# Optimization experiments

Hardware: AMD Instinct MI355X
Metric: run time of the kernel (lower is better)

## Reference

```python
import jax, jax.numpy as jnp
import numpy as np

N_NODES = 20000
N_EDGES = 320000
N_GRAPHS = 64
IN_DIM = 39
HID = 128
HEADS = 4
NUM_CONV = 3
PRED_HID = 32
N_TASKS = 1
NEG_SLOPE = 0.2


def setup_inputs() -> dict:
    key = jax.random.key(0)
    ks = jax.random.split(key, 16)
    node_feat = jax.random.normal(ks[0], (N_NODES, IN_DIM), dtype=jnp.float32)
    edge_index = jax.random.randint(ks[1], (2, N_EDGES), 0, N_NODES, dtype=jnp.int64)
    batch = jnp.sort(jax.random.randint(ks[2], (N_NODES,), 0, N_GRAPHS, dtype=jnp.int64))
    s = 0.05
    return {
        "node_feat": node_feat,
        "edge_index": edge_index,
        "batch": batch,
        "emb_W": jax.random.normal(ks[3], (IN_DIM, HID), dtype=jnp.float32) * s,
        "emb_b": jnp.zeros((HID,), dtype=jnp.float32),
        "lin_W": jax.random.normal(ks[4], (NUM_CONV, HID, HEADS * HID), dtype=jnp.float32) * s,
        "att_src": jax.random.normal(ks[5], (NUM_CONV, HEADS, HID), dtype=jnp.float32) * s,
        "att_dst": jax.random.normal(ks[6], (NUM_CONV, HEADS, HID), dtype=jnp.float32) * s,
        "conv_b": jnp.zeros((NUM_CONV, HID), dtype=jnp.float32),
        "fc_W": jax.random.normal(ks[7], (HID, PRED_HID), dtype=jnp.float32) * s,
        "fc_b": jnp.zeros((PRED_HID,), dtype=jnp.float32),
        "out_W": jax.random.normal(ks[8], (PRED_HID, N_TASKS), dtype=jnp.float32) * s,
        "out_b": jnp.zeros((N_TASKS,), dtype=jnp.float32),
    }


def _gat_layer(x, src, dst, W, a_src, a_dst, b):
    # PyG GATConv (concat=False): per-head projection, additive attention,
    # segment softmax over incoming edges of each target node, head-mean + bias.
    N = x.shape[0]
    h = (x @ W).reshape(N, HEADS, HID)            # [N, H, F]
    a_s = jnp.einsum('nhf,hf->nh', h, a_src)       # [N, H]
    a_d = jnp.einsum('nhf,hf->nh', h, a_dst)       # [N, H]
    e = jax.nn.leaky_relu(a_s[src] + a_d[dst], NEG_SLOPE)   # [E, H]
    e_max = jax.ops.segment_max(e, dst, num_segments=N)      # [N, H]
    e = jnp.exp(e - e_max[dst])
    denom = jax.ops.segment_sum(e, dst, num_segments=N)      # [N, H]
    alpha = e / denom[dst]                                    # [E, H]
    msg = h[src] * alpha[..., None]                           # [E, H, F]
    out = jax.ops.segment_sum(msg, dst, num_segments=N)      # [N, H, F]
    return out.mean(axis=1) + b                               # [N, F]


def reference(node_feat, edge_index, batch, emb_W, emb_b, lin_W, att_src, att_dst,
              conv_b, fc_W, fc_b, out_W, out_b):
    N = node_feat.shape[0]
    loops = jnp.arange(N, dtype=edge_index.dtype)
    src = jnp.concatenate([edge_index[0], loops])  # add_self_loops=True
    dst = jnp.concatenate([edge_index[1], loops])

    x = node_feat @ emb_W + emb_b
    for l in range(NUM_CONV):
        x = _gat_layer(x, src, dst, lin_W[l], att_src[l], att_dst[l], conv_b[l])

    # global_mean_pool
    sums = jax.ops.segment_sum(x, batch, num_segments=N_GRAPHS)              # [G, F]
    cnt = jax.ops.segment_sum(jnp.ones((N,), x.dtype), batch, num_segments=N_GRAPHS)
    g = sums / jnp.maximum(cnt, 1.0)[:, None]

    g = g @ fc_W + fc_b
    return g @ out_W + out_b
```

## Files before the change

kernel.cpp:

```cpp
#include <hip/hip_runtime.h>
#include <math.h>

#define N_NODES 20000
#define E0      320000
#define E_TOT   (E0 + N_NODES)
#define N_GRAPHS 64
#define IN_DIM  39
#define HID     128
#define HEADS   4
#define HHID    (HEADS * HID)
#define NUM_CONV 3
#define PRED_HID 32
#define NEG_SLOPE 0.2f

__device__ __forceinline__ int esrc(const int* __restrict__ ei, int e) {
    return e < E0 ? ei[e] : (e - E0);
}
__device__ __forceinline__ int edst(const int* __restrict__ ei, int e) {
    return e < E0 ? ei[E0 + e] : (e - E0);
}

__global__ void k_deg(const int* __restrict__ ei, int* __restrict__ deg) {
    int e = blockIdx.x * blockDim.x + threadIdx.x;
    if (e >= E_TOT) return;
    atomicAdd(&deg[edst(ei, e)], 1);
}

__global__ __launch_bounds__(1024) void k_scan(const int* __restrict__ deg,
                                               int* __restrict__ row_ptr,
                                               int* __restrict__ cursor) {
    __shared__ int part[1024];
    const int CHUNK = 20;
    int t = threadIdx.x;
    int base = t * CHUNK;
    int s = 0;
    for (int i = 0; i < CHUNK; i++) {
        int idx = base + i;
        if (idx < N_NODES) s += deg[idx];
    }
    part[t] = s;
    __syncthreads();
    for (int off = 1; off < 1024; off <<= 1) {
        int v = (t >= off) ? part[t - off] : 0;
        __syncthreads();
        part[t] += v;
        __syncthreads();
    }
    int run = part[t] - s;
    for (int i = 0; i < CHUNK; i++) {
        int idx = base + i;
        if (idx < N_NODES) {
            row_ptr[idx] = run;
            cursor[idx]  = run;
            run += deg[idx];
        }
    }
    if (t == 1023) row_ptr[N_NODES] = part[1023];
}

__global__ void k_scatter(const int* __restrict__ ei, int* __restrict__ cursor,
                          int* __restrict__ csr_src) {
    int e = blockIdx.x * blockDim.x + threadIdx.x;
    if (e >= E_TOT) return;
    int d = edst(ei, e);
    int pos = atomicAdd(&cursor[d], 1);
    csr_src[pos] = esrc(ei, e);
}

__global__ __launch_bounds__(128) void k_emb(const float* __restrict__ nf,
                                             const float* __restrict__ W,
                                             const float* __restrict__ b,
                                             float* __restrict__ x) {
    __shared__ float f[IN_DIM];
    int n = blockIdx.x, t = threadIdx.x;
    if (t < IN_DIM) f[t] = nf[(size_t)n * IN_DIM + t];
    __syncthreads();
    float acc = b[t];
#pragma unroll
    for (int k = 0; k < IN_DIM; k++) acc += f[k] * W[k * HID + t];
    x[(size_t)n * HID + t] = acc;
}

__global__ __launch_bounds__(128) void k_wsd(const float* __restrict__ lin_W,
                                             const float* __restrict__ attS,
                                             const float* __restrict__ attD,
                                             float* __restrict__ Wsd) {
    int l = blockIdx.x >> 3, j = blockIdx.x & 7, k = threadIdx.x;
    int h = j & 3;
    const float* Wl = lin_W + (size_t)l * HID * HHID;
    const float* av = ((j < 4) ? attS : attD) + ((size_t)l * HEADS + h) * HID;
    const float* wr = Wl + (size_t)k * HHID + h * HID;
    float dot = 0.f;
#pragma unroll 4
    for (int f = 0; f < HID; f++) dot += wr[f] * av[f];
    Wsd[(size_t)l * 8 * HID + j * HID + k] = dot;
}

__global__ __launch_bounds__(256) void k_attproj(const float* __restrict__ x,
                                                 const float* __restrict__ WsdL,
                                                 float* __restrict__ A8) {
    __shared__ float sW[8 * HID];
    for (int i = threadIdx.x; i < 8 * HID; i += 256) sW[i] = WsdL[i];
    __syncthreads();
    int wid = threadIdx.x >> 6, lane = threadIdx.x & 63;
    int n = blockIdx.x * 4 + wid;
    if (n >= N_NODES) return;
    float2 xv = *(const float2*)(x + (size_t)n * HID + lane * 2);
    float p[8];
#pragma unroll
    for (int j = 0; j < 8; j++) {
        float v = xv.x * sW[j * HID + lane * 2] + xv.y * sW[j * HID + lane * 2 + 1];
#pragma unroll
        for (int off = 32; off; off >>= 1) v += __shfl_xor(v, off, 64);
        p[j] = v;
    }
    if (lane == 0) {
        *(float4*)(A8 + (size_t)n * 8)     = make_float4(p[0], p[1], p[2], p[3]);
        *(float4*)(A8 + (size_t)n * 8 + 4) = make_float4(p[4], p[5], p[6], p[7]);
    }
}

__global__ __launch_bounds__(256) void k_aggr(const float* __restrict__ x,
                                              const int* __restrict__ row_ptr,
                                              const int* __restrict__ csr_src,
                                              const float* __restrict__ A8,
                                              float* __restrict__ agg) {
    int wid = threadIdx.x >> 6, lane = threadIdx.x & 63;
    int n = blockIdx.x * 4 + wid;
    if (n >= N_NODES) return;
    float4 vd = *(const float4*)(A8 + (size_t)n * 8 + 4);
    int beg = row_ptr[n], end = row_ptr[n + 1];
    float a0x = 0.f, a0y = 0.f, a1x = 0.f, a1y = 0.f;
    float a2x = 0.f, a2y = 0.f, a3x = 0.f, a3y = 0.f;
    float d0 = 0.f, d1 = 0.f, d2 = 0.f, d3 = 0.f;
    int s_cur = (beg < end) ? csr_src[beg] : 0;
    for (int i = beg; i < end; i++) {
        int s_nx = (i + 1 < end) ? csr_src[i + 1] : 0;
        float4 vs = *(const float4*)(A8 + (size_t)s_cur * 8);
        float2 xv = *(const float2*)(x + (size_t)s_cur * HID + lane * 2);
        float v0 = vs.x + vd.x; v0 = fmaxf(v0, NEG_SLOPE * v0); float e0 = expf(v0);
        float v1 = vs.y + vd.y; v1 = fmaxf(v1, NEG_SLOPE * v1); float e1 = expf(v1);
        float v2 = vs.z + vd.z; v2 = fmaxf(v2, NEG_SLOPE * v2); float e2 = expf(v2);
        float v3 = vs.w + vd.w; v3 = fmaxf(v3, NEG_SLOPE * v3); float e3 = expf(v3);
        a0x += e0 * xv.x; a0y += e0 * xv.y;
        a1x += e1 * xv.x; a1y += e1 * xv.y;
        a2x += e2 * xv.x; a2y += e2 * xv.y;
        a3x += e3 * xv.x; a3y += e3 * xv.y;
        d0 += e0; d1 += e1; d2 += e2; d3 += e3;
        s_cur = s_nx;
    }
    float i0 = 1.f / d0, i1 = 1.f / d1, i2 = 1.f / d2, i3 = 1.f / d3;
    float* ag = agg + (size_t)n * HHID;
    *(float2*)(ag + 0 * HID + lane * 2) = make_float2(a0x * i0, a0y * i0);
    *(float2*)(ag + 1 * HID + lane * 2) = make_float2(a1x * i1, a1y * i1);
    *(float2*)(ag + 2 * HID + lane * 2) = make_float2(a2x * i2, a2y * i2);
    *(float2*)(ag + 3 * HID + lane * 2) = make_float2(a3x * i3, a3y * i3);
}

#define G2_BM 64
#define G2_KSPLIT 4
__global__ __launch_bounds__(256) void k_gemm2(const float* __restrict__ agg,
                                               const float* __restrict__ W,
                                               float* __restrict__ part, int M) {
    __shared__ float At[64][G2_BM];
    __shared__ float Bs[64][HID];
    int tid = threadIdx.x;
    int row0 = blockIdx.x * G2_BM;
    int ks = blockIdx.y;
    int ty = tid >> 4, tx = tid & 15;
    int r0 = ty * 4, c0 = tx * 4;
    float acc[4][8] = {};

#pragma unroll
    for (int kt = 0; kt < 2; kt++) {
        int kbase = ks * 128 + kt * 64;
        __syncthreads();
#pragma unroll
        for (int i = 0; i < 4; i++) {
            int idx = tid + i * 256;
            int r = idx >> 4;
            int c4 = idx & 15;
            int gr = row0 + r;
            float4 v = make_float4(0.f, 0.f, 0.f, 0.f);
            if (gr < M) v = *(const float4*)(agg + (size_t)gr * HHID + kbase + c4 * 4);
            int sw = (((r >> 2) ^ c4) << 2) + (r & 3);
            At[c4 * 4 + 0][sw] = v.x;
            At[c4 * 4 + 1][sw] = v.y;
            At[c4 * 4 + 2][sw] = v.z;
            At[c4 * 4 + 3][sw] = v.w;
        }
#pragma unroll
        for (int i = 0; i < 8; i++) {
            int idx = tid + i * 256;
            int kr = idx >> 5;
            int c4 = idx & 31;
            int kg = kbase + kr;
            int hd = kg >> 7, kk = kg & 127;
            *(float4*)(&Bs[kr][c4 * 4]) =
                *(const float4*)(W + (size_t)kk * HHID + hd * HID + c4 * 4);
        }
        __syncthreads();
#pragma unroll 4
        for (int k = 0; k < 64; k++) {
            float4 av = *(float4*)(&At[k][((ty ^ (k >> 2)) << 2)]);
            float4 b1 = *(float4*)(&Bs[k][c0]);
            float4 b2 = *(float4*)(&Bs[k][c0 + 64]);
            acc[0][0] += av.x * b1.x; acc[0][1] += av.x * b1.y; acc[0][2] += av.x * b1.z; acc[0][3] += av.x * b1.w;
            acc[0][4] += av.x * b2.x; acc[0][5] += av.x * b2.y; acc[0][6] += av.x * b2.z; acc[0][7] += av.x * b2.w;
            acc[1][0] += av.y * b1.x; acc[1][1] += av.y * b1.y; acc[1][2] += av.y * b1.z; acc[1][3] += av.y * b1.w;
            acc[1][4] += av.y * b2.x; acc[1][5] += av.y * b2.y; acc[1][6] += av.y * b2.z; acc[1][7] += av.y * b2.w;
            acc[2][0] += av.z * b1.x; acc[2][1] += av.z * b1.y; acc[2][2] += av.z * b1.z; acc[2][3] += av.z * b1.w;
            acc[2][4] += av.z * b2.x; acc[2][5] += av.z * b2.y; acc[2][6] += av.z * b2.z; acc[2][7] += av.z * b2.w;
            acc[3][0] += av.w * b1.x; acc[3][1] += av.w * b1.y; acc[3][2] += av.w * b1.z; acc[3][3] += av.w * b1.w;
            acc[3][4] += av.w * b2.x; acc[3][5] += av.w * b2.y; acc[3][6] += av.w * b2.z; acc[3][7] += av.w * b2.w;
        }
    }
    float* pb = part + (size_t)ks * M * HID;
#pragma unroll
    for (int i = 0; i < 4; i++) {
        int gr = row0 + r0 + i;
        if (gr < M) {
            *(float4*)(pb + (size_t)gr * HID + c0) =
                make_float4(acc[i][0], acc[i][1], acc[i][2], acc[i][3]);
            *(float4*)(pb + (size_t)gr * HID + c0 + 64) =
                make_float4(acc[i][4], acc[i][5], acc[i][6], acc[i][7]);
        }
    }
}

__global__ __launch_bounds__(256) void k_gfin(const float* __restrict__ part,
                                              const float* __restrict__ bias,
                                              const float* __restrict__ WsdL,
                                              float* __restrict__ xn,
                                              float* __restrict__ A8, int M) {
    __shared__ float sW[8 * HID];
    for (int i = threadIdx.x; i < 8 * HID; i += 256) sW[i] = WsdL[i];
    __syncthreads();
    int wid = threadIdx.x >> 6, lane = threadIdx.x & 63;
    int n = blockIdx.x * 4 + wid;
    if (n >= M) return;
    size_t off = (size_t)n * HID + lane * 2;
    size_t str = (size_t)M * HID;
    float2 p0 = *(const float2*)(part + off);
    float2 p1 = *(const float2*)(part + str + off);
    float2 p2 = *(const float2*)(part + 2 * str + off);
    float2 p3 = *(const float2*)(part + 3 * str + off);
    float2 bb = *(const float2*)(bias + lane * 2);
    float2 xv;
    xv.x = 0.25f * (p0.x + p1.x + p2.x + p3.x) + bb.x;
    xv.y = 0.25f * (p0.y + p1.y + p2.y + p3.y) + bb.y;
    *(float2*)(xn + off) = xv;
    float p[8];
#pragma unroll
    for (int j = 0; j < 8; j++) {
        float v = xv.x * sW[j * HID + lane * 2] + xv.y * sW[j * HID + lane * 2 + 1];
#pragma unroll
        for (int o = 32; o; o >>= 1) v += __shfl_xor(v, o, 64);
        p[j] = v;
    }
    if (lane == 0) {
        *(float4*)(A8 + (size_t)n * 8)     = make_float4(p[0], p[1], p[2], p[3]);
        *(float4*)(A8 + (size_t)n * 8 + 4) = make_float4(p[4], p[5], p[6], p[7]);
    }
}

#define POOL_NPB 64
__global__ __launch_bounds__(128) void k_pool(const float* __restrict__ x,
                                              const int* __restrict__ batch,
                                              float* __restrict__ g_sum,
                                              int* __restrict__ g_cnt) {
    int t = threadIdx.x;
    int n0 = blockIdx.x * POOL_NPB;
    int n1 = n0 + POOL_NPB; if (n1 > N_NODES) n1 = N_NODES;
    if (n0 >= n1) return;
    int cur = batch[n0];
    float acc = 0.f;
    int cnt = 0;
    for (int n = n0; n < n1; n++) {
        int b = batch[n];
        if (b != cur) {
            atomicAdd(&g_sum[cur * HID + t], acc);
            if (t == 0) atomicAdd(&g_cnt[cur], cnt);
            acc = 0.f; cnt = 0; cur = b;
        }
        acc += x[(size_t)n * HID + t];
        cnt++;
    }
    atomicAdd(&g_sum[cur * HID + t], acc);
    if (t == 0) atomicAdd(&g_cnt[cur], cnt);
}

__global__ __launch_bounds__(64) void k_head(const float* __restrict__ g_sum,
                                             const int* __restrict__ g_cnt,
                                             const float* __restrict__ fcW,
                                             const float* __restrict__ fcb,
                                             const float* __restrict__ outW,
                                             const float* __restrict__ outb,
                                             float* __restrict__ out) {
    int g = blockIdx.x, t = threadIdx.x;
    float inv = 1.f / fmaxf((float)g_cnt[g], 1.f);
    float val = 0.f;
    if (t < PRED_HID) {
        float dot = fcb[t];
        for (int f = 0; f < HID; f++)
            dot += (g_sum[g * HID + f] * inv) * fcW[f * PRED_HID + t];
        val = dot * outW[t];
    }
#pragma unroll
    for (int off = 32; off; off >>= 1) val += __shfl_xor(val, off, 64);
    if (t == 0) out[g] = val + outb[0];
}

extern "C" void kernel_launch(void* const* d_in, const int* in_sizes, int n_in,
                              void* d_out, int out_size, void* d_ws, size_t ws_size,
                              hipStream_t stream) {
    const float* node_feat = (const float*)d_in[0];
    const int*   edge_index = (const int*)d_in[1];
    const int*   batch     = (const int*)d_in[2];
    const float* emb_W     = (const float*)d_in[3];
    const float* emb_b     = (const float*)d_in[4];
    const float* lin_W     = (const float*)d_in[5];
    const float* att_src   = (const float*)d_in[6];
    const float* att_dst   = (const float*)d_in[7];
    const float* conv_b    = (const float*)d_in[8];
    const float* fc_W      = (const float*)d_in[9];
    const float* fc_b      = (const float*)d_in[10];
    const float* out_W     = (const float*)d_in[11];
    const float* out_b     = (const float*)d_in[12];
    float* out = (float*)d_out;

    char* p = (char*)d_ws;
    auto alloc = [&](size_t bytes) {
        void* r = (void*)p;
        p += (bytes + 255) & ~(size_t)255;
        return r;
    };
    float* x0      = (float*)alloc((size_t)N_NODES * HID * 4);
    float* x1      = (float*)alloc((size_t)N_NODES * HID * 4);
    float* agg     = (float*)alloc((size_t)N_NODES * HHID * 4);
    float* part    = (float*)alloc((size_t)G2_KSPLIT * N_NODES * HID * 4);
    float* A8      = (float*)alloc((size_t)N_NODES * 8 * 4);
    float* Wsd     = (float*)alloc((size_t)NUM_CONV * 8 * HID * 4);
    int*   deg     = (int*)alloc((size_t)(N_NODES + 1) * 4);
    int*   row_ptr = (int*)alloc((size_t)(N_NODES + 1) * 4);
    int*   cursor  = (int*)alloc((size_t)N_NODES * 4);
    int*   csr_src = (int*)alloc((size_t)E_TOT * 4);
    float* g_sum   = (float*)alloc((size_t)N_GRAPHS * HID * 4);
    int*   g_cnt   = (int*)alloc((size_t)N_GRAPHS * 4);

    const int EB = (E_TOT + 255) / 256;
    const int NB4 = (N_NODES + 3) / 4;

    hipMemsetAsync(deg, 0, (size_t)N_NODES * 4, stream);
    k_deg<<<EB, 256, 0, stream>>>(edge_index, deg);
    k_scan<<<1, 1024, 0, stream>>>(deg, row_ptr, cursor);
    k_scatter<<<EB, 256, 0, stream>>>(edge_index, cursor, csr_src);

    k_wsd<<<NUM_CONV * 8, 128, 0, stream>>>(lin_W, att_src, att_dst, Wsd);

    k_emb<<<N_NODES, 128, 0, stream>>>(node_feat, emb_W, emb_b, x0);
    k_attproj<<<NB4, 256, 0, stream>>>(x0, Wsd, A8);

    float* xin = x0;
    float* xout = x1;
    for (int l = 0; l < NUM_CONV; l++) {
        const float* Wl = lin_W + (size_t)l * HID * HHID;
        const float* bl = conv_b + (size_t)l * HID;
        int lnext = (l + 1 < NUM_CONV) ? l + 1 : NUM_CONV - 1;

        k_aggr<<<NB4, 256, 0, stream>>>(xin, row_ptr, csr_src, A8, agg);
        dim3 gg((N_NODES + G2_BM - 1) / G2_BM, G2_KSPLIT);
        k_gemm2<<<gg, 256, 0, stream>>>(agg, Wl, part, N_NODES);
        k_gfin<<<NB4, 256, 0, stream>>>(part, bl, Wsd + (size_t)lnext * 8 * HID,
                                        xout, A8, N_NODES);
        float* tmp = xin; xin = xout; xout = tmp;
    }

    hipMemsetAsync(g_sum, 0, (size_t)N_GRAPHS * HID * 4, stream);
    hipMemsetAsync(g_cnt, 0, (size_t)N_GRAPHS * 4, stream);
    k_pool<<<(N_NODES + POOL_NPB - 1) / POOL_NPB, 128, 0, stream>>>(xin, batch, g_sum, g_cnt);
    k_head<<<N_GRAPHS, 64, 0, stream>>>(g_sum, g_cnt, fc_W, fc_b,
                                        out_W, out_b, out);
}
```

Measured before the change: 480.3 us.

## Precompute per-edge attention exponentials in a separate edge kernel

Adds a per-edge kernel that computes the leaky-relu and exp of the attention logits once per edge per head and stores them in CSR order, using a new csr_dst array written during scatter. Before this, each of the 64 lanes in a wave computed those exps redundantly. The aggregation kernel now reads the precomputed values and prefetches the next edge's weights and source features one iteration ahead. The cost is an extra launch per layer plus writing and re-reading about 5 MB of edge weights.

New measurement: 456.4 us. 1.05x faster.

```diff
diff --git a/kernel.cpp b/kernel.cpp
--- a/kernel.cpp
+++ b/kernel.cpp
@@ -59,12 +59,13 @@
 }
 
 __global__ void k_scatter(const int* __restrict__ ei, int* __restrict__ cursor,
-                          int* __restrict__ csr_src) {
+                          int* __restrict__ csr_src, int* __restrict__ csr_dst) {
     int e = blockIdx.x * blockDim.x + threadIdx.x;
     if (e >= E_TOT) return;
     int d = edst(ei, e);
     int pos = atomicAdd(&cursor[d], 1);
     csr_src[pos] = esrc(ei, e);
+    csr_dst[pos] = d;
 }
 
 __global__ __launch_bounds__(128) void k_emb(const float* __restrict__ nf,
@@ -120,34 +121,54 @@
     }
 }
 
+__global__ void k_edge(const int* __restrict__ csr_src, const int* __restrict__ csr_dst,
+                       const float* __restrict__ A8, float* __restrict__ expE) {
+    int j = blockIdx.x * blockDim.x + threadIdx.x;
+    if (j >= E_TOT) return;
+    int s = csr_src[j], d = csr_dst[j];
+    float4 vs = *(const float4*)(A8 + (size_t)s * 8);
+    float4 vd = *(const float4*)(A8 + (size_t)d * 8 + 4);
+    float4 r;
+    float v;
+    v = vs.x + vd.x; v = fmaxf(v, NEG_SLOPE * v); r.x = expf(v);
+    v = vs.y + vd.y; v = fmaxf(v, NEG_SLOPE * v); r.y = expf(v);
+    v = vs.z + vd.z; v = fmaxf(v, NEG_SLOPE * v); r.z = expf(v);
+    v = vs.w + vd.w; v = fmaxf(v, NEG_SLOPE * v); r.w = expf(v);
+    *(float4*)(expE + (size_t)j * HEADS) = r;
+}
+
 __global__ __launch_bounds__(256) void k_aggr(const float* __restrict__ x,
                                               const int* __restrict__ row_ptr,
                                               const int* __restrict__ csr_src,
-                                              const float* __restrict__ A8,
+                                              const float* __restrict__ expE,
                                               float* __restrict__ agg) {
     int wid = threadIdx.x >> 6, lane = threadIdx.x & 63;
     int n = blockIdx.x * 4 + wid;
     if (n >= N_NODES) return;
-    float4 vd = *(const float4*)(A8 + (size_t)n * 8 + 4);
     int beg = row_ptr[n], end = row_ptr[n + 1];
     float a0x = 0.f, a0y = 0.f, a1x = 0.f, a1y = 0.f;
     float a2x = 0.f, a2y = 0.f, a3x = 0.f, a3y = 0.f;
     float d0 = 0.f, d1 = 0.f, d2 = 0.f, d3 = 0.f;
-    int s_cur = (beg < end) ? csr_src[beg] : 0;
+    float4 ep_nx = make_float4(0.f, 0.f, 0.f, 0.f);
+    float2 xv_nx = make_float2(0.f, 0.f);
+    if (beg < end) {
+        int s0 = csr_src[beg];
+        ep_nx = *(const float4*)(expE + (size_t)beg * HEADS);
+        xv_nx = *(const float2*)(x + (size_t)s0 * HID + lane * 2);
+    }
     for (int i = beg; i < end; i++) {
-        int s_nx = (i + 1 < end) ? csr_src[i + 1] : 0;
-        float4 vs = *(const float4*)(A8 + (size_t)s_cur * 8);
-        float2 xv = *(const float2*)(x + (size_t)s_cur * HID + lane * 2);
-        float v0 = vs.x + vd.x; v0 = fmaxf(v0, NEG_SLOPE * v0); float e0 = expf(v0);
-        float v1 = vs.y + vd.y; v1 = fmaxf(v1, NEG_SLOPE * v1); float e1 = expf(v1);
-        float v2 = vs.z + vd.z; v2 = fmaxf(v2, NEG_SLOPE * v2); float e2 = expf(v2);
-        float v3 = vs.w + vd.w; v3 = fmaxf(v3, NEG_SLOPE * v3); float e3 = expf(v3);
-        a0x += e0 * xv.x; a0y += e0 * xv.y;
-        a1x += e1 * xv.x; a1y += e1 * xv.y;
-        a2x += e2 * xv.x; a2y += e2 * xv.y;
-        a3x += e3 * xv.x; a3y += e3 * xv.y;
-        d0 += e0; d1 += e1; d2 += e2; d3 += e3;
-        s_cur = s_nx;
+        float4 ep = ep_nx;
+        float2 xv = xv_nx;
+        if (i + 1 < end) {
+            int s2 = csr_src[i + 1];
+            ep_nx = *(const float4*)(expE + (size_t)(i + 1) * HEADS);
+            xv_nx = *(const float2*)(x + (size_t)s2 * HID + lane * 2);
+        }
+        a0x += ep.x * xv.x; a0y += ep.x * xv.y;
+        a1x += ep.y * xv.x; a1y += ep.y * xv.y;
+        a2x += ep.z * xv.x; a2y += ep.z * xv.y;
+        a3x += ep.w * xv.x; a3y += ep.w * xv.y;
+        d0 += ep.x; d1 += ep.y; d2 += ep.z; d3 += ep.w;
     }
     float i0 = 1.f / d0, i1 = 1.f / d1, i2 = 1.f / d2, i3 = 1.f / d3;
     float* ag = agg + (size_t)n * HHID;
@@ -341,10 +362,12 @@
     float* part    = (float*)alloc((size_t)G2_KSPLIT * N_NODES * HID * 4);
     float* A8      = (float*)alloc((size_t)N_NODES * 8 * 4);
     float* Wsd     = (float*)alloc((size_t)NUM_CONV * 8 * HID * 4);
+    float* expE    = (float*)alloc((size_t)E_TOT * HEADS * 4);
     int*   deg     = (int*)alloc((size_t)(N_NODES + 1) * 4);
     int*   row_ptr = (int*)alloc((size_t)(N_NODES + 1) * 4);
     int*   cursor  = (int*)alloc((size_t)N_NODES * 4);
     int*   csr_src = (int*)alloc((size_t)E_TOT * 4);
+    int*   csr_dst = (int*)alloc((size_t)E_TOT * 4);
     float* g_sum   = (float*)alloc((size_t)N_GRAPHS * HID * 4);
     int*   g_cnt   = (int*)alloc((size_t)N_GRAPHS * 4);
 
@@ -354,7 +377,7 @@
     hipMemsetAsync(deg, 0, (size_t)N_NODES * 4, stream);
     k_deg<<<EB, 256, 0, stream>>>(edge_index, deg);
     k_scan<<<1, 1024, 0, stream>>>(deg, row_ptr, cursor);
-    k_scatter<<<EB, 256, 0, stream>>>(edge_index, cursor, csr_src);
+    k_scatter<<<EB, 256, 0, stream>>>(edge_index, cursor, csr_src, csr_dst);
 
     k_wsd<<<NUM_CONV * 8, 128, 0, stream>>>(lin_W, att_src, att_dst, Wsd);
 
@@ -368,7 +391,8 @@
         const float* bl = conv_b + (size_t)l * HID;
         int lnext = (l + 1 < NUM_CONV) ? l + 1 : NUM_CONV - 1;
 
-        k_aggr<<<NB4, 256, 0, stream>>>(xin, row_ptr, csr_src, A8, agg);
+        k_edge<<<EB, 256, 0, stream>>>(csr_src, csr_dst, A8, expE);
+        k_aggr<<<NB4, 256, 0, stream>>>(xin, row_ptr, csr_src, expE, agg);
         dim3 gg((N_NODES + G2_BM - 1) / G2_BM, G2_KSPLIT);
         k_gemm2<<<gg, 256, 0, stream>>>(agg, Wl, part, N_NODES);
         k_gfin<<<NB4, 256, 0, stream>>>(part, bl, Wsd + (size_t)lnext * 8 * HID,
```
